# Kernel optimization log

Measured on AMD Instinct MI355X. Metric: run time of the kernel, lower is better.

The kernel has to match this reference:

```python
import jax, jax.numpy as jnp
import numpy as np

B, T, D, H, L = 2048, 512, 8, 20, 10  # batch, seq, input_dim, hidden_dim, num_layers


def setup_inputs() -> dict:
    key = jax.random.key(0)
    ks = jax.random.split(key, 10)
    s = 1.0 / np.sqrt(H)  # PyTorch nn.RNN / nn.Linear init bound
    u = lambda k, shape: jax.random.uniform(k, shape, jnp.float32, -s, s)
    return {
        "x": jax.random.normal(ks[0], (B, T, D), jnp.float32),
        "w_ih0": u(ks[1], (H, D)),        # layer-0 input weights
        "w_ih": u(ks[2], (L - 1, H, H)),  # layers 1..9 input weights
        "w_hh": u(ks[3], (L, H, H)),
        "b_ih": u(ks[4], (L, H)),
        "b_hh": u(ks[5], (L, H)),
        "fc_w": u(ks[6], (H, H)),
        "fc_b": u(ks[7], (H,)),
        "l2_w": u(ks[8], (1, H)),
        "l2_b": u(ks[9], (1,)),
    }


def reference(x, w_ih0, w_ih, w_hh, b_ih, b_hh, fc_w, fc_b, l2_w, l2_b):
    # 10-layer Elman RNN (tanh), batch_first, h0 = 0, eval mode (no dropout).
    Bn = x.shape[0]
    h0 = jnp.zeros((L, Bn, H), x.dtype)

    def step(h, x_t):  # h: [L, B, H], x_t: [B, D]
        hs = []
        inp = x_t
        for l in range(L):  # fixed small layer count -> unrolled
            Wi = w_ih0 if l == 0 else w_ih[l - 1]
            hl = jnp.tanh(inp @ Wi.T + b_ih[l] + h[l] @ w_hh[l].T + b_hh[l])
            hs.append(hl)
            inp = hl
        return jnp.stack(hs), hl  # carry, top-layer output

    _, out = jax.lax.scan(step, h0, jnp.swapaxes(x, 0, 1))  # out: [T, B, H]
    out = jnp.swapaxes(out, 0, 1)  # [B, T, H]
    # Time-independent MLP head (original loops over t; batched here, same math)
    y = jax.nn.relu(out @ fc_w.T + fc_b) @ l2_w.T + l2_b  # [B, T, 1]
    return y
```

## Files before the change

### kernel.cpp

```cpp
#include <hip/hip_runtime.h>

#if __has_builtin(__builtin_amdgcn_exp2f)
#define EXP2F(x) __builtin_amdgcn_exp2f(x)
#else
#define EXP2F(x) exp2f(x)
#endif
#if __has_builtin(__builtin_amdgcn_rcpf)
#define RCPF(x) __builtin_amdgcn_rcpf(x)
#else
#define RCPF(x) (1.0f / (x))
#endif

namespace {

constexpr int B_ = 2048, T_ = 512, D_ = 8, H_ = 20, L_ = 10;
constexpr int NG   = 16;
constexpr int PADK = 40;
constexpr int NW   = 11;
constexpr int NTHR = NW * 64;
constexpr int NDIAG = T_ + L_;

typedef float f32x4 __attribute__((ext_vector_type(4)));
typedef short s16x8 __attribute__((ext_vector_type(8)));

#define LD4(p) (*reinterpret_cast<const f32x4*>(p))

__device__ __forceinline__ unsigned short f2bf(float f) {
    unsigned u = __builtin_bit_cast(unsigned, f);
    return (unsigned short)((u + 0x7FFFu + ((u >> 16) & 1u)) >> 16);
}
__device__ __forceinline__ float bf2f(unsigned short b) {
    return __builtin_bit_cast(float, (unsigned)b << 16);
}

__device__ __forceinline__ f32x4 mfma_bf16(s16x8 a, s16x8 b, f32x4 c) {
    return __builtin_amdgcn_mfma_f32_16x16x32_bf16(a, b, c, 0, 0, 0);
}

__device__ __forceinline__ float tanh_fast(float x) {
    float e = EXP2F(x * 2.8853900817779268f);
    return fmaf(-2.0f, RCPF(1.0f + e), 1.0f);
}

__global__ __launch_bounds__(NTHR) void rnn_mfma(
    const float* __restrict__ x,
    const float* __restrict__ w_ih0,
    const float* __restrict__ w_ih,
    const float* __restrict__ w_hh,
    const float* __restrict__ b_ih,
    const float* __restrict__ b_hh,
    const float* __restrict__ fc_w,
    const float* __restrict__ fc_b,
    const float* __restrict__ l2_w,
    const float* __restrict__ l2_b,
    float* __restrict__ out)
{
    __shared__ __align__(16) unsigned short h_lds[2][L_][NG][PADK];

    const int tid = threadIdx.x;
    const int w   = tid >> 6;
    const int l   = tid & 63;
    const int col = l & 15;
    const int g   = l >> 4;
    const int bg  = blockIdx.x * NG;

    for (int i = tid; i < 2 * L_ * NG * PADK; i += NTHR)
        (&h_lds[0][0][0][0])[i] = 0;

    s16x8 a0_hi = {0,0,0,0,0,0,0,0}, a0_lo = a0_hi, a1_hi = a0_hi, a1_lo = a0_hi;
    s16x8 h0_hi = a0_hi, h0_lo = a0_hi, h1_hi = a0_hi, h1_lo = a0_hi;
    f32x4 bias0 = {0.f, 0.f, 0.f, 0.f}, bias1 = bias0;
    f32x4 l2v0 = bias0, l2v1 = bias0;
    float l2bv = 0.f;
    const bool mt1ok = col < (H_ - 16);

    if (w < L_) {
        const int layer = w;
        #pragma unroll
        for (int e = 0; e < 8; ++e) {
            const int k = g * 8 + e;
            float wv0 = 0.f, wv1 = 0.f;
            if (layer == 0) {
                if (k < 16) {
                    wv0 = w_ih0[col * D_ + (k & 7)];
                    if (mt1ok) wv1 = w_ih0[(16 + col) * D_ + (k & 7)];
                }
            } else if (k < H_) {
                wv0 = w_ih[((layer - 1) * H_ + col) * H_ + k];
                if (mt1ok) wv1 = w_ih[((layer - 1) * H_ + 16 + col) * H_ + k];
            }
            unsigned short b0 = f2bf(wv0), b1 = f2bf(wv1);
            a0_hi[e] = (short)b0; a0_lo[e] = (short)f2bf(wv0 - bf2f(b0));
            a1_hi[e] = (short)b1; a1_lo[e] = (short)f2bf(wv1 - bf2f(b1));
            float uv0 = 0.f, uv1 = 0.f;
            if (k < H_) {
                uv0 = w_hh[(layer * H_ + col) * H_ + k];
                if (mt1ok) uv1 = w_hh[(layer * H_ + 16 + col) * H_ + k];
            }
            unsigned short c0 = f2bf(uv0), c1 = f2bf(uv1);
            h0_hi[e] = (short)c0; h0_lo[e] = (short)f2bf(uv0 - bf2f(c0));
            h1_hi[e] = (short)c1; h1_lo[e] = (short)f2bf(uv1 - bf2f(c1));
        }
        #pragma unroll
        for (int r = 0; r < 4; ++r) {
            const int row = g * 4 + r;
            bias0[r] = b_ih[layer * H_ + row] + b_hh[layer * H_ + row];
            bias1[r] = (g == 0) ? (b_ih[layer * H_ + 16 + r] +
                                   b_hh[layer * H_ + 16 + r]) : 0.f;
        }
    } else {
        #pragma unroll
        for (int e = 0; e < 8; ++e) {
            const int k = g * 8 + e;
            float f0 = 0.f, f1 = 0.f;
            if (k < H_) {
                f0 = fc_w[col * H_ + k];
                if (mt1ok) f1 = fc_w[(16 + col) * H_ + k];
            }
            unsigned short b0 = f2bf(f0), b1 = f2bf(f1);
            a0_hi[e] = (short)b0; a0_lo[e] = (short)f2bf(f0 - bf2f(b0));
            a1_hi[e] = (short)b1; a1_lo[e] = (short)f2bf(f1 - bf2f(b1));
        }
        #pragma unroll
        for (int r = 0; r < 4; ++r) {
            bias0[r] = fc_b[g * 4 + r];
            bias1[r] = (g == 0) ? fc_b[16 + r] : 0.f;
            l2v0[r]  = l2_w[g * 4 + r];
            l2v1[r]  = (g == 0) ? l2_w[16 + r] : 0.f;
        }
        l2bv = l2_b[0];
    }

    f32x4 xa_n = {0.f, 0.f, 0.f, 0.f}, xb_n = xa_n;
    if (w == 0 && g < 2) {
        const float* xp = x + (size_t)(bg + col) * T_ * D_;
        xa_n = LD4(xp); xb_n = LD4(xp + 4);
    }
    __syncthreads();

    for (int c = 0; c < NDIAG; ++c) {
        const int cur = c & 1, prv = cur ^ 1;

        if (w < L_) {
            const int t = c - w;
            if ((unsigned)t < (unsigned)T_) {
                s16x8 B0;
                if (w == 0) {
                    s16x8 xf = {0,0,0,0,0,0,0,0};
                    if (g < 2) {
                        #pragma unroll
                        for (int e = 0; e < 8; ++e) {
                            float f = (e < 4) ? xa_n[e] : xb_n[e - 4];
                            unsigned short hb = f2bf(f);
                            xf[e] = (short)((g == 0) ? hb : f2bf(f - bf2f(hb)));
                        }
                        if (t + 1 < T_) {
                            const float* xp = x + ((size_t)(bg + col) * T_ + t + 1) * D_;
                            xa_n = LD4(xp); xb_n = LD4(xp + 4);
                        }
                    }
                    B0 = xf;
                } else {
                    B0 = *reinterpret_cast<const s16x8*>(&h_lds[prv][w - 1][col][g * 8]);
                }
                s16x8 B1 = *reinterpret_cast<const s16x8*>(&h_lds[prv][w][col][g * 8]);
                f32x4 acc0 = bias0, acc1 = bias1;
                acc0 = mfma_bf16(a0_hi, B0, acc0);
                acc0 = mfma_bf16(a0_lo, B0, acc0);
                acc0 = mfma_bf16(h0_hi, B1, acc0);
                acc0 = mfma_bf16(h0_lo, B1, acc0);
                acc1 = mfma_bf16(a1_hi, B0, acc1);
                acc1 = mfma_bf16(a1_lo, B0, acc1);
                acc1 = mfma_bf16(h1_hi, B1, acc1);
                acc1 = mfma_bf16(h1_lo, B1, acc1);
                unsigned p0 = (unsigned)f2bf(tanh_fast(acc0[0])) |
                              ((unsigned)f2bf(tanh_fast(acc0[1])) << 16);
                unsigned p1 = (unsigned)f2bf(tanh_fast(acc0[2])) |
                              ((unsigned)f2bf(tanh_fast(acc0[3])) << 16);
                *reinterpret_cast<uint2*>(&h_lds[cur][w][col][g * 4]) =
                    make_uint2(p0, p1);
                if (g == 0) {
                    unsigned q0 = (unsigned)f2bf(tanh_fast(acc1[0])) |
                                  ((unsigned)f2bf(tanh_fast(acc1[1])) << 16);
                    unsigned q1 = (unsigned)f2bf(tanh_fast(acc1[2])) |
                                  ((unsigned)f2bf(tanh_fast(acc1[3])) << 16);
                    *reinterpret_cast<uint2*>(&h_lds[cur][w][col][16]) =
                        make_uint2(q0, q1);
                }
            }
        } else {
            const int th = c - L_;
            if ((unsigned)th < (unsigned)T_) {
                s16x8 Bh = *reinterpret_cast<const s16x8*>(&h_lds[prv][L_ - 1][col][g * 8]);
                f32x4 z0 = bias0, z1 = bias1;
                z0 = mfma_bf16(a0_hi, Bh, z0);
                z0 = mfma_bf16(a0_lo, Bh, z0);
                z1 = mfma_bf16(a1_hi, Bh, z1);
                z1 = mfma_bf16(a1_lo, Bh, z1);
                float part = 0.f;
                #pragma unroll
                for (int r = 0; r < 4; ++r) {
                    part = fmaf(l2v0[r], fmaxf(z0[r], 0.f), part);
                    part = fmaf(l2v1[r], fmaxf(z1[r], 0.f), part);
                }
                part += __shfl_xor(part, 16);
                part += __shfl_xor(part, 32);
                if (l < NG) out[(size_t)(bg + l) * T_ + th] = part + l2bv;
            }
        }
        __syncthreads();
    }
}

}

extern "C" void kernel_launch(void* const* d_in, const int* in_sizes, int n_in,
                              void* d_out, int out_size, void* d_ws, size_t ws_size,
                              hipStream_t stream) {
    const float* x     = (const float*)d_in[0];
    const float* w_ih0 = (const float*)d_in[1];
    const float* w_ih  = (const float*)d_in[2];
    const float* w_hh  = (const float*)d_in[3];
    const float* b_ih  = (const float*)d_in[4];
    const float* b_hh  = (const float*)d_in[5];
    const float* fc_w  = (const float*)d_in[6];
    const float* fc_b  = (const float*)d_in[7];
    const float* l2_w  = (const float*)d_in[8];
    const float* l2_b  = (const float*)d_in[9];
    float* out = (float*)d_out;

    const int grid = B_ / NG;
    hipLaunchKernelGGL(rnn_mfma, dim3(grid), dim3(NTHR), 0, stream,
                       x, w_ih0, w_ih, w_hh, b_ih, b_hh, fc_w, fc_b,
                       l2_w, l2_b, out);
}
```

Baseline: 390.0 us.

## Replace per-diagonal block barriers with per-wave LDS progress counters and 4-slot ring

Drops the wavefront-diagonal loop and its __syncthreads after every step. Each wave now runs its own time loop and spins on workgroup-scope atomic progress counters in LDS, so a layer waits only on the layer below and, through a 4-deep ring of hidden-state slots, on the layer above for slot reuse. It also splits the MFMA chains into independent hi/lo accumulators for more instruction-level parallelism, uses v_cvt_pk_bf16_f32 for packing, and prefetches x two steps ahead. The risks are spin-wait cost and the correctness of the memory ordering.

```diff
diff --git a/kernel.cpp b/kernel.cpp
--- a/kernel.cpp
+++ b/kernel.cpp
@@ -14,11 +14,13 @@
 namespace {
 
 constexpr int B_ = 2048, T_ = 512, D_ = 8, H_ = 20, L_ = 10;
-constexpr int NG   = 16;
-constexpr int PADK = 40;
-constexpr int NW   = 11;
-constexpr int NTHR = NW * 64;
-constexpr int NDIAG = T_ + L_;
+constexpr int NG    = 16;
+constexpr int PADK  = 40;
+constexpr int NW    = 11;
+constexpr int NTHR  = NW * 64;
+constexpr int DEPTH = 4;
+constexpr int SLOT_STRIDE  = L_ * NG * PADK;
+constexpr int LAYER_STRIDE = NG * PADK;
 
 typedef float f32x4 __attribute__((ext_vector_type(4)));
 typedef short s16x8 __attribute__((ext_vector_type(8)));
@@ -32,6 +34,11 @@
 __device__ __forceinline__ float bf2f(unsigned short b) {
     return __builtin_bit_cast(float, (unsigned)b << 16);
 }
+__device__ __forceinline__ unsigned cvt_pk_bf16(float s0, float s1) {
+    unsigned r;
+    asm("v_cvt_pk_bf16_f32 %0, %1, %2" : "=v"(r) : "v"(s0), "v"(s1));
+    return r;
+}
 
 __device__ __forceinline__ f32x4 mfma_bf16(s16x8 a, s16x8 b, f32x4 c) {
     return __builtin_amdgcn_mfma_f32_16x16x32_bf16(a, b, c, 0, 0, 0);
@@ -42,7 +49,13 @@
     return fmaf(-2.0f, RCPF(1.0f + e), 1.0f);
 }
 
-__global__ __launch_bounds__(NTHR) void rnn_mfma(
+__device__ __forceinline__ void wait_ge(int* p, int v) {
+    while (__hip_atomic_load(p, __ATOMIC_ACQUIRE,
+                             __HIP_MEMORY_SCOPE_WORKGROUP) < v) {}
+    __builtin_amdgcn_sched_barrier(0);
+}
+
+__global__ __launch_bounds__(NTHR) void rnn_async(
     const float* __restrict__ x,
     const float* __restrict__ w_ih0,
     const float* __restrict__ w_ih,
@@ -55,7 +68,8 @@
     const float* __restrict__ l2_b,
     float* __restrict__ out)
 {
-    __shared__ __align__(16) unsigned short h_lds[2][L_][NG][PADK];
+    __shared__ __align__(16) unsigned short h_lds[DEPTH][L_][NG][PADK];
+    __shared__ int prog[16];
 
     const int tid = threadIdx.x;
     const int w   = tid >> 6;
@@ -64,8 +78,12 @@
     const int g   = l >> 4;
     const int bg  = blockIdx.x * NG;
 
-    for (int i = tid; i < 2 * L_ * NG * PADK; i += NTHR)
-        (&h_lds[0][0][0][0])[i] = 0;
+    {
+        uint4* p4 = reinterpret_cast<uint4*>(&h_lds[0][0][0][0]);
+        const int n4 = DEPTH * L_ * NG * PADK / 8;
+        for (int i = tid; i < n4; i += NTHR) p4[i] = make_uint4(0, 0, 0, 0);
+        if (tid < 16) prog[tid] = 0;
+    }
 
     s16x8 a0_hi = {0,0,0,0,0,0,0,0}, a0_lo = a0_hi, a1_hi = a0_hi, a1_lo = a0_hi;
     s16x8 h0_hi = a0_hi, h0_lo = a0_hi, h1_hi = a0_hi, h1_lo = a0_hi;
@@ -131,84 +149,95 @@
         l2bv = l2_b[0];
     }
 
-    f32x4 xa_n = {0.f, 0.f, 0.f, 0.f}, xb_n = xa_n;
+    f32x4 xc0 = {0.f,0.f,0.f,0.f}, xc1 = xc0, xn0 = xc0, xn1 = xc0;
     if (w == 0 && g < 2) {
         const float* xp = x + (size_t)(bg + col) * T_ * D_;
-        xa_n = LD4(xp); xb_n = LD4(xp + 4);
-    }
+        xc0 = LD4(xp);      xc1 = LD4(xp + 4);
+        xn0 = LD4(xp + D_); xn1 = LD4(xp + D_ + 4);
+    }
+
     __syncthreads();
 
-    for (int c = 0; c < NDIAG; ++c) {
-        const int cur = c & 1, prv = cur ^ 1;
-
-        if (w < L_) {
-            const int t = c - w;
-            if ((unsigned)t < (unsigned)T_) {
-                s16x8 B0;
-                if (w == 0) {
-                    s16x8 xf = {0,0,0,0,0,0,0,0};
-                    if (g < 2) {
-                        #pragma unroll
-                        for (int e = 0; e < 8; ++e) {
-                            float f = (e < 4) ? xa_n[e] : xb_n[e - 4];
-                            unsigned short hb = f2bf(f);
-                            xf[e] = (short)((g == 0) ? hb : f2bf(f - bf2f(hb)));
-                        }
-                        if (t + 1 < T_) {
-                            const float* xp = x + ((size_t)(bg + col) * T_ + t + 1) * D_;
-                            xa_n = LD4(xp); xb_n = LD4(xp + 4);
-                        }
+    unsigned short* const hb = &h_lds[0][0][0][0];
+    const f32x4 z4 = {0.f, 0.f, 0.f, 0.f};
+
+    if (w < L_) {
+        const int rdB1 = w * LAYER_STRIDE + col * PADK + g * 8;
+        const int rdB0 = (w ? (w - 1) * LAYER_STRIDE : 0) + col * PADK + g * 8;
+        const int wr0  = w * LAYER_STRIDE + col * PADK + g * 4;
+        const int wr1  = w * LAYER_STRIDE + col * PADK + 16;
+        for (int t = 0; t < T_; ++t) {
+            const int s_cur = (t & 3) * SLOT_STRIDE;
+            const int s_prv = ((t + 3) & 3) * SLOT_STRIDE;
+            s16x8 B1 = *reinterpret_cast<const s16x8*>(hb + s_prv + rdB1);
+            if (t >= DEPTH) wait_ge(&prog[w + 1], t - (DEPTH - 1));
+            s16x8 B0;
+            if (w == 0) {
+                s16x8 xf = {0,0,0,0,0,0,0,0};
+                if (g < 2) {
+                    #pragma unroll
+                    for (int e = 0; e < 8; ++e) {
+                        float f = (e < 4) ? xc0[e] : xc1[e - 4];
+                        unsigned short hbit = f2bf(f);
+                        xf[e] = (short)((g == 0) ? hbit : f2bf(f - bf2f(hbit)));
                     }
-                    B0 = xf;
-                } else {
-                    B0 = *reinterpret_cast<const s16x8*>(&h_lds[prv][w - 1][col][g * 8]);
+                    xc0 = xn0; xc1 = xn1;
+                    if (t + 2 < T_) {
+                        const float* xp = x + ((size_t)(bg + col) * T_ + t + 2) * D_;
+                        xn0 = LD4(xp); xn1 = LD4(xp + 4);
+                    }
                 }
-                s16x8 B1 = *reinterpret_cast<const s16x8*>(&h_lds[prv][w][col][g * 8]);
-                f32x4 acc0 = bias0, acc1 = bias1;
-                acc0 = mfma_bf16(a0_hi, B0, acc0);
-                acc0 = mfma_bf16(a0_lo, B0, acc0);
-                acc0 = mfma_bf16(h0_hi, B1, acc0);
-                acc0 = mfma_bf16(h0_lo, B1, acc0);
-                acc1 = mfma_bf16(a1_hi, B0, acc1);
-                acc1 = mfma_bf16(a1_lo, B0, acc1);
-                acc1 = mfma_bf16(h1_hi, B1, acc1);
-                acc1 = mfma_bf16(h1_lo, B1, acc1);
-                unsigned p0 = (unsigned)f2bf(tanh_fast(acc0[0])) |
-                              ((unsigned)f2bf(tanh_fast(acc0[1])) << 16);
-                unsigned p1 = (unsigned)f2bf(tanh_fast(acc0[2])) |
-                              ((unsigned)f2bf(tanh_fast(acc0[3])) << 16);
-                *reinterpret_cast<uint2*>(&h_lds[cur][w][col][g * 4]) =
-                    make_uint2(p0, p1);
-                if (g == 0) {
-                    unsigned q0 = (unsigned)f2bf(tanh_fast(acc1[0])) |
-                                  ((unsigned)f2bf(tanh_fast(acc1[1])) << 16);
-                    unsigned q1 = (unsigned)f2bf(tanh_fast(acc1[2])) |
-                                  ((unsigned)f2bf(tanh_fast(acc1[3])) << 16);
-                    *reinterpret_cast<uint2*>(&h_lds[cur][w][col][16]) =
-                        make_uint2(q0, q1);
-                }
-            }
-        } else {
-            const int th = c - L_;
-            if ((unsigned)th < (unsigned)T_) {
-                s16x8 Bh = *reinterpret_cast<const s16x8*>(&h_lds[prv][L_ - 1][col][g * 8]);
-                f32x4 z0 = bias0, z1 = bias1;
-                z0 = mfma_bf16(a0_hi, Bh, z0);
-                z0 = mfma_bf16(a0_lo, Bh, z0);
-                z1 = mfma_bf16(a1_hi, Bh, z1);
-                z1 = mfma_bf16(a1_lo, Bh, z1);
-                float part = 0.f;
-                #pragma unroll
-                for (int r = 0; r < 4; ++r) {
-                    part = fmaf(l2v0[r], fmaxf(z0[r], 0.f), part);
-                    part = fmaf(l2v1[r], fmaxf(z1[r], 0.f), part);
-                }
-                part += __shfl_xor(part, 16);
-                part += __shfl_xor(part, 32);
-                if (l < NG) out[(size_t)(bg + l) * T_ + th] = part + l2bv;
-            }
-        }
-        __syncthreads();
+                B0 = xf;
+            } else {
+                wait_ge(&prog[w - 1], t + 1);
+                B0 = *reinterpret_cast<const s16x8*>(hb + s_cur + rdB0);
+            }
+            f32x4 A  = mfma_bf16(h0_hi, B1, bias0);
+            f32x4 Ab = mfma_bf16(h0_lo, B1, z4);
+            f32x4 C  = mfma_bf16(h1_hi, B1, bias1);
+            f32x4 Cb = mfma_bf16(h1_lo, B1, z4);
+            A  = mfma_bf16(a0_hi, B0, A);
+            Ab = mfma_bf16(a0_lo, B0, Ab);
+            C  = mfma_bf16(a1_hi, B0, C);
+            Cb = mfma_bf16(a1_lo, B0, Cb);
+            f32x4 acc0 = A + Ab, acc1 = C + Cb;
+            uint2 pw;
+            pw.x = cvt_pk_bf16(tanh_fast(acc0[0]), tanh_fast(acc0[1]));
+            pw.y = cvt_pk_bf16(tanh_fast(acc0[2]), tanh_fast(acc0[3]));
+            *reinterpret_cast<uint2*>(hb + s_cur + wr0) = pw;
+            if (g == 0) {
+                uint2 qw;
+                qw.x = cvt_pk_bf16(tanh_fast(acc1[0]), tanh_fast(acc1[1]));
+                qw.y = cvt_pk_bf16(tanh_fast(acc1[2]), tanh_fast(acc1[3]));
+                *reinterpret_cast<uint2*>(hb + s_cur + wr1) = qw;
+            }
+            if (l == 0)
+                __hip_atomic_store(&prog[w], t + 1, __ATOMIC_RELEASE,
+                                   __HIP_MEMORY_SCOPE_WORKGROUP);
+        }
+    } else {
+        const int rdH = (L_ - 1) * LAYER_STRIDE + col * PADK + g * 8;
+        for (int t = 0; t < T_; ++t) {
+            wait_ge(&prog[L_ - 1], t + 1);
+            s16x8 Bh = *reinterpret_cast<const s16x8*>(
+                hb + (t & 3) * SLOT_STRIDE + rdH);
+            f32x4 z0 = mfma_bf16(a0_hi, Bh, bias0);
+            z0 = mfma_bf16(a0_lo, Bh, z0);
+            f32x4 z1 = mfma_bf16(a1_hi, Bh, bias1);
+            z1 = mfma_bf16(a1_lo, Bh, z1);
+            float part = 0.f;
+            #pragma unroll
+            for (int r = 0; r < 4; ++r) {
+                part = fmaf(l2v0[r], fmaxf(z0[r], 0.f), part);
+                part = fmaf(l2v1[r], fmaxf(z1[r], 0.f), part);
+            }
+            part += __shfl_xor(part, 16);
+            part += __shfl_xor(part, 32);
+            if (l < NG) out[(size_t)(bg + l) * T_ + t] = part + l2bv;
+            if (l == 0)
+                __hip_atomic_store(&prog[L_], t + 1, __ATOMIC_RELEASE,
+                                   __HIP_MEMORY_SCOPE_WORKGROUP);
+        }
     }
 }
 
@@ -230,7 +259,7 @@
     float* out = (float*)d_out;
 
     const int grid = B_ / NG;
-    hipLaunchKernelGGL(rnn_mfma, dim3(grid), dim3(NTHR), 0, stream,
+    hipLaunchKernelGGL(rnn_async, dim3(grid), dim3(NTHR), 0, stream,
                        x, w_ih0, w_ih, w_hh, b_ih, b_hh, fc_w, fc_b,
                        l2_w, l2_b, out);
 }
```

New measurement: 357.3 us. 8.4% less time.
